# Optimization experiments

Hardware: AMD Instinct MI355X
Metric: run time of the kernel (lower is better)

## Reference

```python
import jax, jax.numpy as jnp
import numpy as np

N = 50000
E = 800000
D_IN = 256
D_OUT = 256
ALPHA = 0.5


def setup_inputs() -> dict:
    key = jax.random.key(0)
    k1, k2, k3, k4, k5, k6 = jax.random.split(key, 6)
    stdv = 1.0 / np.sqrt(D_OUT)
    return {
        "input": jax.random.normal(k1, (N, D_IN), dtype=jnp.float32),
        "adj_src": jax.random.randint(k2, (E,), 0, N, dtype=jnp.int64),
        "adj_dst": jax.random.randint(k3, (E,), 0, N, dtype=jnp.int64),
        "adj_w": jax.random.uniform(k4, (E,), dtype=jnp.float32),
        "init_input": jax.random.normal(k5, (N, D_OUT), dtype=jnp.float32),
        "weight": jax.random.uniform(k6, (D_IN, D_OUT), dtype=jnp.float32,
                                     minval=-stdv, maxval=stdv),
    }


def reference(input, adj_src, adj_dst, adj_w, init_input, weight):
    # support = input @ W          [N, D_OUT] (dense GEMM)
    support = jnp.matmul(input, weight)
    # spmm: out[dst] += w * support[src]   (COO aggregate)
    msgs = support[adj_src] * adj_w[:, None]          # [E, D_OUT]
    agg = jax.ops.segment_sum(msgs, adj_dst, num_segments=N)  # [N, D_OUT]
    # alpha-blended residual + ReLU (bias=False, act=ReLU)
    out = agg * ALPHA + init_input * (1.0 - ALPHA)
    return jax.nn.relu(out)
```

## Files before the change

### kernel.cpp

```cpp
#include <hip/hip_runtime.h>
#include <hip/hip_fp16.h>

#define ALPHA 0.5f

typedef short short8v __attribute__((ext_vector_type(8)));
typedef float f32x4 __attribute__((ext_vector_type(4)));

__device__ __forceinline__ unsigned short f2bf(float f) {
  union { float f; unsigned u; } v; v.f = f;
  unsigned r = v.u + 0x7FFFu + ((v.u >> 16) & 1u);
  return (unsigned short)(r >> 16);
}
__device__ __forceinline__ float bf2f(unsigned short u) {
  union { unsigned u; float f; } v; v.u = ((unsigned)u) << 16;
  return v.f;
}
__device__ __forceinline__ float unpack_w(unsigned p) {
  return __half2float(__ushort_as_half((unsigned short)((p & 0x7FFFu) << 1)));
}

__global__ __launch_bounds__(256) void prep_small(
    const float* __restrict__ W, unsigned short* __restrict__ Wt,
    int* __restrict__ deg, int* __restrict__ scanmeta, int N) {
  const int tid = threadIdx.x;
  const int bid = blockIdx.x;
  if (bid < 256) {
    __shared__ float tile[16][17];
    const int kb = (bid & 15) * 16, nb = (bid >> 4) * 16;
    const int tx = tid & 15, ty = tid >> 4;
    tile[ty][tx] = W[(kb + ty) * 256 + nb + tx];
    __syncthreads();
    Wt[(nb + ty) * 256 + kb + tx] = f2bf(tile[tx][ty]);
  } else {
    if (bid == 256 && tid < 128) scanmeta[tid] = 0;
    const int base = ((bid - 256) * 256 + tid) * 4;
    if (base + 3 < N) *reinterpret_cast<int4*>(&deg[base]) = make_int4(0, 0, 0, 0);
    else for (int j = 0; j < 4; ++j) if (base + j < N) deg[base + j] = 0;
  }
}

__global__ __launch_bounds__(256) void gemm_hist(
    const float* __restrict__ A, const unsigned short* __restrict__ Wt,
    unsigned short* __restrict__ C, int M,
    const int* __restrict__ dst, int* __restrict__ deg, int E,
    const float* __restrict__ init, unsigned short* __restrict__ init_bf, int n8i,
    int GB, int HB, int CB) {
  __shared__ char smem[2][24576];
  const int tid = threadIdx.x;
  const int bid = blockIdx.x;

  if (bid >= GB + HB) {
    const int cgid = (bid - GB - HB) * 256 + tid;
    const int cstride = CB * 256;
    for (int i = cgid; i < n8i; i += cstride) {
      float4 a = *reinterpret_cast<const float4*>(&init[i * 8]);
      float4 b = *reinterpret_cast<const float4*>(&init[i * 8 + 4]);
      unsigned short o[8] = {
        f2bf(a.x * (1.f - ALPHA)), f2bf(a.y * (1.f - ALPHA)),
        f2bf(a.z * (1.f - ALPHA)), f2bf(a.w * (1.f - ALPHA)),
        f2bf(b.x * (1.f - ALPHA)), f2bf(b.y * (1.f - ALPHA)),
        f2bf(b.z * (1.f - ALPHA)), f2bf(b.w * (1.f - ALPHA))};
      *reinterpret_cast<short8v*>(&init_bf[i * 8]) = *reinterpret_cast<short8v*>(o);
    }
    return;
  }
  if (bid >= GB) {
    const int hgid = (bid - GB) * 256 + tid;
    const int hstride = HB * 256;
    const int E4 = E & ~3;
    for (int i = hgid * 4; i < E4; i += hstride * 4) {
      int4 d = *reinterpret_cast<const int4*>(&dst[i]);
      atomicAdd(&deg[d.x], 1); atomicAdd(&deg[d.y], 1);
      atomicAdd(&deg[d.z], 1); atomicAdd(&deg[d.w], 1);
    }
    if (hgid < (E - E4)) atomicAdd(&deg[dst[E4 + hgid]], 1);
    return;
  }

  const int lane = tid & 63;
  const int w = tid >> 6;
  const int wm = w >> 1, wn = w & 1;
  const int row0 = bid * 128;

  f32x4 acc[4][8];
  #pragma unroll
  for (int m = 0; m < 4; ++m)
    #pragma unroll
    for (int n = 0; n < 8; ++n) acc[m][n] = (f32x4){0.f, 0.f, 0.f, 0.f};

  const int aR = tid >> 1;
  const int aKs = (tid & 1) * 16;
  const int aRow = (row0 + aR < M) ? (row0 + aR) : (M - 1);
  const float* aP = A + (size_t)aRow * 256 + aKs;
  const int aWrOff = (aR >> 4) * 1024 + (aKs >> 3) * 256 + (aR & 15) * 16;

  int cur = 0;
  {
    float4 av[4];
    #pragma unroll
    for (int j = 0; j < 4; ++j) av[j] = *reinterpret_cast<const float4*>(aP + j * 4);
    #pragma unroll
    for (int i = 0; i < 4; ++i) {
      int s = w * 4 + i;
      const unsigned short* g = Wt + (size_t)(s * 16 + (lane & 15)) * 256 + (lane >> 4) * 8;
      __builtin_amdgcn_global_load_lds(
          (const __attribute__((address_space(1))) void*)g,
          (__attribute__((address_space(3))) void*)(&smem[0][8192 + s * 1024]),
          16, 0, 0);
    }
    unsigned short ab[16];
    #pragma unroll
    for (int j = 0; j < 4; ++j) {
      ab[j * 4 + 0] = f2bf(av[j].x); ab[j * 4 + 1] = f2bf(av[j].y);
      ab[j * 4 + 2] = f2bf(av[j].z); ab[j * 4 + 3] = f2bf(av[j].w);
    }
    *reinterpret_cast<short8v*>(&smem[0][aWrOff])       = *reinterpret_cast<short8v*>(&ab[0]);
    *reinterpret_cast<short8v*>(&smem[0][aWrOff + 256]) = *reinterpret_cast<short8v*>(&ab[8]);
    __syncthreads();
  }

  #pragma unroll
  for (int t = 0; t < 8; ++t) {
    float4 av[4];
    const bool pf = (t < 7);
    if (pf) {
      const int k0 = (t + 1) * 32;
      #pragma unroll
      for (int j = 0; j < 4; ++j) av[j] = *reinterpret_cast<const float4*>(aP + k0 + j * 4);
      #pragma unroll
      for (int i = 0; i < 4; ++i) {
        int s = w * 4 + i;
        const unsigned short* g = Wt + (size_t)(s * 16 + (lane & 15)) * 256 + k0 + (lane >> 4) * 8;
        __builtin_amdgcn_global_load_lds(
            (const __attribute__((address_space(1))) void*)g,
            (__attribute__((address_space(3))) void*)(&smem[cur ^ 1][8192 + s * 1024]),
            16, 0, 0);
      }
    }
    short8v af[4], bfv[8];
    #pragma unroll
    for (int m = 0; m < 4; ++m)
      af[m] = *reinterpret_cast<const short8v*>(&smem[cur][(wm * 4 + m) * 1024 + lane * 16]);
    #pragma unroll
    for (int n = 0; n < 8; ++n)
      bfv[n] = *reinterpret_cast<const short8v*>(&smem[cur][8192 + (wn * 8 + n) * 1024 + lane * 16]);
    #pragma unroll
    for (int m = 0; m < 4; ++m)
      #pragma unroll
      for (int n = 0; n < 8; ++n)
        acc[m][n] = __builtin_amdgcn_mfma_f32_16x16x32_bf16(af[m], bfv[n], acc[m][n], 0, 0, 0);
    if (pf) {
      unsigned short ab[16];
      #pragma unroll
      for (int j = 0; j < 4; ++j) {
        ab[j * 4 + 0] = f2bf(av[j].x); ab[j * 4 + 1] = f2bf(av[j].y);
        ab[j * 4 + 2] = f2bf(av[j].z); ab[j * 4 + 3] = f2bf(av[j].w);
      }
      *reinterpret_cast<short8v*>(&smem[cur ^ 1][aWrOff])       = *reinterpret_cast<short8v*>(&ab[0]);
      *reinterpret_cast<short8v*>(&smem[cur ^ 1][aWrOff + 256]) = *reinterpret_cast<short8v*>(&ab[8]);
    }
    __syncthreads();
    cur ^= 1;
  }

  #pragma unroll
  for (int m = 0; m < 4; ++m) {
    #pragma unroll
    for (int n = 0; n < 8; ++n) {
      const int col = wn * 128 + n * 16 + (lane & 15);
      #pragma unroll
      for (int r = 0; r < 4; ++r) {
        const int row = row0 + wm * 64 + m * 16 + (lane >> 4) * 4 + r;
        if (row < M) C[(size_t)row * 256 + col] = f2bf(acc[m][n][r]);
      }
    }
  }
}

__global__ __launch_bounds__(256) void scan_lookback(
    const int* __restrict__ deg, int* __restrict__ row_ptr, int* __restrict__ cursor,
    int* __restrict__ scanmeta ,
    int N, int E, int NB) {
  int* flags = scanmeta;
  int* aggv  = scanmeta + 64;
  const int tid = threadIdx.x;
  const int bid = blockIdx.x;
  const int base = bid * 1024 + tid * 4;

  int4 v = make_int4(0, 0, 0, 0);
  if (base + 3 < N) v = *reinterpret_cast<const int4*>(&deg[base]);
  else {
    if (base + 0 < N) v.x = deg[base + 0];
    if (base + 1 < N) v.y = deg[base + 1];
    if (base + 2 < N) v.z = deg[base + 2];
  }
  const int s = v.x + v.y + v.z + v.w;
  const int lane = tid & 63, wid = tid >> 6;
  int ps = s;
  #pragma unroll
  for (int off = 1; off < 64; off <<= 1) {
    int t = __shfl_up(ps, off, 64);
    if (lane >= off) ps += t;
  }
  __shared__ int wsum[4];
  __shared__ int s_off;
  if (lane == 63) wsum[wid] = ps;
  __syncthreads();
  int woff = 0;
  #pragma unroll
  for (int w2 = 0; w2 < 4; ++w2) woff += (w2 < wid) ? wsum[w2] : 0;
  const int texcl = woff + ps - s;

  if (tid == 0) {
    int total = wsum[0] + wsum[1] + wsum[2] + wsum[3];
    atomicExch(&aggv[bid], total);
    __threadfence();
    atomicExch(&flags[bid], 1);
  }
  if (bid == 0 && tid == 0) row_ptr[N] = E;

  if (tid < 64) {
    int a = 0;
    if (tid < bid) {
      while (atomicAdd(&flags[tid], 0) == 0) { }
      a = atomicAdd(&aggv[tid], 0);
    }
    #pragma unroll
    for (int m = 1; m < 64; m <<= 1) a += __shfl_xor(a, m, 64);
    if (tid == 0) s_off = a;
  }
  __syncthreads();
  const int off = s_off;

  int4 e = make_int4(texcl + off, texcl + off + v.x,
                     texcl + off + v.x + v.y, texcl + off + v.x + v.y + v.z);
  if (base + 3 < N) {
    *reinterpret_cast<int4*>(&row_ptr[base]) = e;
    *reinterpret_cast<int4*>(&cursor[base]) = e;
  } else {
    int ev[4] = {e.x, e.y, e.z, e.w};
    for (int j = 0; j < 4; ++j)
      if (base + j < N) { row_ptr[base + j] = ev[j]; cursor[base + j] = ev[j]; }
  }
}

__global__ __launch_bounds__(256) void reindex_edges(
    const int* __restrict__ src, const int* __restrict__ dst,
    const float* __restrict__ w, int* __restrict__ cursor,
    unsigned* __restrict__ edges, int E) {
  int i = (blockIdx.x * blockDim.x + threadIdx.x) * 4;
  if (i + 3 < E) {
    int4 sv = *reinterpret_cast<const int4*>(&src[i]);
    int4 dv = *reinterpret_cast<const int4*>(&dst[i]);
    float4 wv = *reinterpret_cast<const float4*>(&w[i]);
    int s_[4] = {sv.x, sv.y, sv.z, sv.w};
    int d_[4] = {dv.x, dv.y, dv.z, dv.w};
    float w_[4] = {wv.x, wv.y, wv.z, wv.w};
    #pragma unroll
    for (int j = 0; j < 4; ++j) {
      int slot = atomicAdd(&cursor[d_[j]], 1);
      unsigned hb = __half_as_ushort(__float2half(w_[j] * ALPHA));
      edges[slot] = ((unsigned)s_[j] << 15) | (hb >> 1);
    }
  } else {
    for (; i < E; ++i) {
      int slot = atomicAdd(&cursor[dst[i]], 1);
      unsigned hb = __half_as_ushort(__float2half(w[i] * ALPHA));
      edges[slot] = ((unsigned)src[i] << 15) | (hb >> 1);
    }
  }
}

__global__ __launch_bounds__(256) void aggregate(
    const unsigned short* __restrict__ support,
    const int* __restrict__ row_ptr,
    const unsigned* __restrict__ edges,
    const unsigned short* __restrict__ init_bf, float* __restrict__ out, int N) {
  int node = blockIdx.x * 4 + (threadIdx.x >> 6);
  if (node >= N) return;
  int lane = threadIdx.x & 63;
  int start = row_ptr[node];
  int cnt = row_ptr[node + 1] - start;

  ushort4 ib = *reinterpret_cast<const ushort4*>(&init_bf[(size_t)node * 256 + lane * 4]);

  float4 acc = make_float4(0.f, 0.f, 0.f, 0.f);
  int e = 0;
  for (; e + 7 < cnt; e += 8) {
    unsigned p[8];
    #pragma unroll
    for (int j = 0; j < 8; ++j) p[j] = edges[start + e + j];
    ushort4 v[8];
    #pragma unroll
    for (int j = 0; j < 8; ++j)
      v[j] = *reinterpret_cast<const ushort4*>(&support[(size_t)(p[j] >> 15) * 256 + lane * 4]);
    #pragma unroll
    for (int j = 0; j < 8; ++j) {
      float wj = unpack_w(p[j]);
      acc.x += wj * bf2f(v[j].x);
      acc.y += wj * bf2f(v[j].y);
      acc.z += wj * bf2f(v[j].z);
      acc.w += wj * bf2f(v[j].w);
    }
  }
  for (; e < cnt; ++e) {
    unsigned p = edges[start + e];
    ushort4 v = *reinterpret_cast<const ushort4*>(&support[(size_t)(p >> 15) * 256 + lane * 4]);
    float wj = unpack_w(p);
    acc.x += wj * bf2f(v.x); acc.y += wj * bf2f(v.y);
    acc.z += wj * bf2f(v.z); acc.w += wj * bf2f(v.w);
  }
  float4 o;
  o.x = fmaxf(acc.x + bf2f(ib.x), 0.f);
  o.y = fmaxf(acc.y + bf2f(ib.y), 0.f);
  o.z = fmaxf(acc.z + bf2f(ib.z), 0.f);
  o.w = fmaxf(acc.w + bf2f(ib.w), 0.f);
  *reinterpret_cast<float4*>(&out[(size_t)node * 256 + lane * 4]) = o;
}

extern "C" void kernel_launch(void* const* d_in, const int* in_sizes, int n_in,
                              void* d_out, int out_size, void* d_ws, size_t ws_size,
                              hipStream_t stream) {
  const float* input   = (const float*)d_in[0];
  const int*   adj_src = (const int*)d_in[1];
  const int*   adj_dst = (const int*)d_in[2];
  const float* adj_w   = (const float*)d_in[3];
  const float* init_in = (const float*)d_in[4];
  const float* weight  = (const float*)d_in[5];
  float* out = (float*)d_out;

  const int N = in_sizes[0] / 256;
  const int E = in_sizes[1];

  char* ws = (char*)d_ws;
  unsigned short* support = (unsigned short*)ws; ws += (size_t)N * 256 * 2;
  unsigned short* init_bf = (unsigned short*)ws; ws += (size_t)N * 256 * 2;
  unsigned short* Wt      = (unsigned short*)ws; ws += 256 * 256 * 2;
  int* deg      = (int*)ws; ws += (size_t)N * 4;
  int* row_ptr  = (int*)ws; ws += (size_t)(N + 1) * 4;
  int* cursor   = (int*)ws; ws += (size_t)N * 4;
  int* scanmeta = (int*)ws; ws += 128 * 4;
  unsigned* edges = (unsigned*)ws; ws += (size_t)E * 4;

  const int NB = (N + 1023) / 1024;
  const int GB = (N + 127) / 128;
  const int HB = 640;
  const int CB = 320;
  const int n8i = N * 256 / 8;

  prep_small<<<256 + (N / 4 + 255) / 256, 256, 0, stream>>>(weight, Wt, deg, scanmeta, N);

  gemm_hist<<<GB + HB + CB, 256, 0, stream>>>(input, Wt, support, N,
                                              adj_dst, deg, E,
                                              init_in, init_bf, n8i, GB, HB, CB);

  scan_lookback<<<NB, 256, 0, stream>>>(deg, row_ptr, cursor, scanmeta, N, E, NB);

  reindex_edges<<<(E / 4 + 255) / 256, 256, 0, stream>>>(adj_src, adj_dst, adj_w, cursor, edges, E);

  aggregate<<<(N + 3) / 4, 256, 0, stream>>>(support, row_ptr, edges, init_bf, out, N);
}
```

Before: 193.7 us.

## Move GEMM from histogram kernel to co-run with edge reindexing

Result: faster. 189.1 us (-2.4%).

```diff
diff --git a/kernel.cpp b/kernel.cpp
--- a/kernel.cpp
+++ b/kernel.cpp
@@ -39,33 +39,15 @@
   }
 }
 
-__global__ __launch_bounds__(256) void gemm_hist(
-    const float* __restrict__ A, const unsigned short* __restrict__ Wt,
-    unsigned short* __restrict__ C, int M,
+__global__ __launch_bounds__(256) void hist_cvt(
     const int* __restrict__ dst, int* __restrict__ deg, int E,
     const float* __restrict__ init, unsigned short* __restrict__ init_bf, int n8i,
-    int GB, int HB, int CB) {
-  __shared__ char smem[2][24576];
+    int HB, int CB) {
   const int tid = threadIdx.x;
   const int bid = blockIdx.x;
 
-  if (bid >= GB + HB) {
-    const int cgid = (bid - GB - HB) * 256 + tid;
-    const int cstride = CB * 256;
-    for (int i = cgid; i < n8i; i += cstride) {
-      float4 a = *reinterpret_cast<const float4*>(&init[i * 8]);
-      float4 b = *reinterpret_cast<const float4*>(&init[i * 8 + 4]);
-      unsigned short o[8] = {
-        f2bf(a.x * (1.f - ALPHA)), f2bf(a.y * (1.f - ALPHA)),
-        f2bf(a.z * (1.f - ALPHA)), f2bf(a.w * (1.f - ALPHA)),
-        f2bf(b.x * (1.f - ALPHA)), f2bf(b.y * (1.f - ALPHA)),
-        f2bf(b.z * (1.f - ALPHA)), f2bf(b.w * (1.f - ALPHA))};
-      *reinterpret_cast<short8v*>(&init_bf[i * 8]) = *reinterpret_cast<short8v*>(o);
-    }
-    return;
-  }
-  if (bid >= GB) {
-    const int hgid = (bid - GB) * 256 + tid;
+  if (bid < HB) {
+    const int hgid = bid * 256 + tid;
     const int hstride = HB * 256;
     const int E4 = E & ~3;
     for (int i = hgid * 4; i < E4; i += hstride * 4) {
@@ -76,104 +58,17 @@
     if (hgid < (E - E4)) atomicAdd(&deg[dst[E4 + hgid]], 1);
     return;
   }
-
-  const int lane = tid & 63;
-  const int w = tid >> 6;
-  const int wm = w >> 1, wn = w & 1;
-  const int row0 = bid * 128;
-
-  f32x4 acc[4][8];
-  #pragma unroll
-  for (int m = 0; m < 4; ++m)
-    #pragma unroll
-    for (int n = 0; n < 8; ++n) acc[m][n] = (f32x4){0.f, 0.f, 0.f, 0.f};
-
-  const int aR = tid >> 1;
-  const int aKs = (tid & 1) * 16;
-  const int aRow = (row0 + aR < M) ? (row0 + aR) : (M - 1);
-  const float* aP = A + (size_t)aRow * 256 + aKs;
-  const int aWrOff = (aR >> 4) * 1024 + (aKs >> 3) * 256 + (aR & 15) * 16;
-
-  int cur = 0;
-  {
-    float4 av[4];
-    #pragma unroll
-    for (int j = 0; j < 4; ++j) av[j] = *reinterpret_cast<const float4*>(aP + j * 4);
-    #pragma unroll
-    for (int i = 0; i < 4; ++i) {
-      int s = w * 4 + i;
-      const unsigned short* g = Wt + (size_t)(s * 16 + (lane & 15)) * 256 + (lane >> 4) * 8;
-      __builtin_amdgcn_global_load_lds(
-          (const __attribute__((address_space(1))) void*)g,
-          (__attribute__((address_space(3))) void*)(&smem[0][8192 + s * 1024]),
-          16, 0, 0);
-    }
-    unsigned short ab[16];
-    #pragma unroll
-    for (int j = 0; j < 4; ++j) {
-      ab[j * 4 + 0] = f2bf(av[j].x); ab[j * 4 + 1] = f2bf(av[j].y);
-      ab[j * 4 + 2] = f2bf(av[j].z); ab[j * 4 + 3] = f2bf(av[j].w);
-    }
-    *reinterpret_cast<short8v*>(&smem[0][aWrOff])       = *reinterpret_cast<short8v*>(&ab[0]);
-    *reinterpret_cast<short8v*>(&smem[0][aWrOff + 256]) = *reinterpret_cast<short8v*>(&ab[8]);
-    __syncthreads();
-  }
-
-  #pragma unroll
-  for (int t = 0; t < 8; ++t) {
-    float4 av[4];
-    const bool pf = (t < 7);
-    if (pf) {
-      const int k0 = (t + 1) * 32;
-      #pragma unroll
-      for (int j = 0; j < 4; ++j) av[j] = *reinterpret_cast<const float4*>(aP + k0 + j * 4);
-      #pragma unroll
-      for (int i = 0; i < 4; ++i) {
-        int s = w * 4 + i;
-        const unsigned short* g = Wt + (size_t)(s * 16 + (lane & 15)) * 256 + k0 + (lane >> 4) * 8;
-        __builtin_amdgcn_global_load_lds(
-            (const __attribute__((address_space(1))) void*)g,
-            (__attribute__((address_space(3))) void*)(&smem[cur ^ 1][8192 + s * 1024]),
-            16, 0, 0);
-      }
-    }
-    short8v af[4], bfv[8];
-    #pragma unroll
-    for (int m = 0; m < 4; ++m)
-      af[m] = *reinterpret_cast<const short8v*>(&smem[cur][(wm * 4 + m) * 1024 + lane * 16]);
-    #pragma unroll
-    for (int n = 0; n < 8; ++n)
-      bfv[n] = *reinterpret_cast<const short8v*>(&smem[cur][8192 + (wn * 8 + n) * 1024 + lane * 16]);
-    #pragma unroll
-    for (int m = 0; m < 4; ++m)
-      #pragma unroll
-      for (int n = 0; n < 8; ++n)
-        acc[m][n] = __builtin_amdgcn_mfma_f32_16x16x32_bf16(af[m], bfv[n], acc[m][n], 0, 0, 0);
-    if (pf) {
-      unsigned short ab[16];
-      #pragma unroll
-      for (int j = 0; j < 4; ++j) {
-        ab[j * 4 + 0] = f2bf(av[j].x); ab[j * 4 + 1] = f2bf(av[j].y);
-        ab[j * 4 + 2] = f2bf(av[j].z); ab[j * 4 + 3] = f2bf(av[j].w);
-      }
-      *reinterpret_cast<short8v*>(&smem[cur ^ 1][aWrOff])       = *reinterpret_cast<short8v*>(&ab[0]);
-      *reinterpret_cast<short8v*>(&smem[cur ^ 1][aWrOff + 256]) = *reinterpret_cast<short8v*>(&ab[8]);
-    }
-    __syncthreads();
-    cur ^= 1;
-  }
-
-  #pragma unroll
-  for (int m = 0; m < 4; ++m) {
-    #pragma unroll
-    for (int n = 0; n < 8; ++n) {
-      const int col = wn * 128 + n * 16 + (lane & 15);
-      #pragma unroll
-      for (int r = 0; r < 4; ++r) {
-        const int row = row0 + wm * 64 + m * 16 + (lane >> 4) * 4 + r;
-        if (row < M) C[(size_t)row * 256 + col] = f2bf(acc[m][n][r]);
-      }
-    }
+  const int cgid = (bid - HB) * 256 + tid;
+  const int cstride = CB * 256;
+  for (int i = cgid; i < n8i; i += cstride) {
+    float4 a = *reinterpret_cast<const float4*>(&init[i * 8]);
+    float4 b = *reinterpret_cast<const float4*>(&init[i * 8 + 4]);
+    unsigned short o[8] = {
+      f2bf(a.x * (1.f - ALPHA)), f2bf(a.y * (1.f - ALPHA)),
+      f2bf(a.z * (1.f - ALPHA)), f2bf(a.w * (1.f - ALPHA)),
+      f2bf(b.x * (1.f - ALPHA)), f2bf(b.y * (1.f - ALPHA)),
+      f2bf(b.z * (1.f - ALPHA)), f2bf(b.w * (1.f - ALPHA))};
+    *reinterpret_cast<short8v*>(&init_bf[i * 8]) = *reinterpret_cast<short8v*>(o);
   }
 }
 
@@ -244,29 +139,138 @@
   }
 }
 
-__global__ __launch_bounds__(256) void reindex_edges(
+__global__ __launch_bounds__(256) void gemm_reindex(
+    const float* __restrict__ A, const unsigned short* __restrict__ Wt,
+    unsigned short* __restrict__ C, int M,
     const int* __restrict__ src, const int* __restrict__ dst,
-    const float* __restrict__ w, int* __restrict__ cursor,
-    unsigned* __restrict__ edges, int E) {
-  int i = (blockIdx.x * blockDim.x + threadIdx.x) * 4;
-  if (i + 3 < E) {
-    int4 sv = *reinterpret_cast<const int4*>(&src[i]);
-    int4 dv = *reinterpret_cast<const int4*>(&dst[i]);
-    float4 wv = *reinterpret_cast<const float4*>(&w[i]);
-    int s_[4] = {sv.x, sv.y, sv.z, sv.w};
-    int d_[4] = {dv.x, dv.y, dv.z, dv.w};
-    float w_[4] = {wv.x, wv.y, wv.z, wv.w};
+    const float* __restrict__ wgt, int* __restrict__ cursor,
+    unsigned* __restrict__ edges, int E, int GB, int RB) {
+  __shared__ char smem[2][24576];
+  const int tid = threadIdx.x;
+  const int bid = blockIdx.x;
+
+  if (bid >= GB) {
+    const int rbid = bid - GB;
+    int i = (rbid * 256 + tid) * 4;
+    if (i + 3 < E) {
+      int4 sv = *reinterpret_cast<const int4*>(&src[i]);
+      int4 dv = *reinterpret_cast<const int4*>(&dst[i]);
+      float4 wv = *reinterpret_cast<const float4*>(&wgt[i]);
+      int s_[4] = {sv.x, sv.y, sv.z, sv.w};
+      int d_[4] = {dv.x, dv.y, dv.z, dv.w};
+      float w_[4] = {wv.x, wv.y, wv.z, wv.w};
+      #pragma unroll
+      for (int j = 0; j < 4; ++j) {
+        int slot = atomicAdd(&cursor[d_[j]], 1);
+        unsigned hb = __half_as_ushort(__float2half(w_[j] * ALPHA));
+        edges[slot] = ((unsigned)s_[j] << 15) | (hb >> 1);
+      }
+    } else {
+      for (; i < E; ++i) {
+        int slot = atomicAdd(&cursor[dst[i]], 1);
+        unsigned hb = __half_as_ushort(__float2half(wgt[i] * ALPHA));
+        edges[slot] = ((unsigned)src[i] << 15) | (hb >> 1);
+      }
+    }
+    return;
+  }
+
+  const int lane = tid & 63;
+  const int w = tid >> 6;
+  const int wm = w >> 1, wn = w & 1;
+  const int row0 = bid * 128;
+
+  f32x4 acc[4][8];
+  #pragma unroll
+  for (int m = 0; m < 4; ++m)
+    #pragma unroll
+    for (int n = 0; n < 8; ++n) acc[m][n] = (f32x4){0.f, 0.f, 0.f, 0.f};
+
+  const int aR = tid >> 1;
+  const int aKs = (tid & 1) * 16;
+  const int aRow = (row0 + aR < M) ? (row0 + aR) : (M - 1);
+  const float* aP = A + (size_t)aRow * 256 + aKs;
+  const int aWrOff = (aR >> 4) * 1024 + (aKs >> 3) * 256 + (aR & 15) * 16;
+
+  int cur = 0;
+  {
+    float4 av[4];
+    #pragma unroll
+    for (int j = 0; j < 4; ++j) av[j] = *reinterpret_cast<const float4*>(aP + j * 4);
+    #pragma unroll
+    for (int i = 0; i < 4; ++i) {
+      int s = w * 4 + i;
+      const unsigned short* g = Wt + (size_t)(s * 16 + (lane & 15)) * 256 + (lane >> 4) * 8;
+      __builtin_amdgcn_global_load_lds(
+          (const __attribute__((address_space(1))) void*)g,
+          (__attribute__((address_space(3))) void*)(&smem[0][8192 + s * 1024]),
+          16, 0, 0);
+    }
+    unsigned short ab[16];
     #pragma unroll
     for (int j = 0; j < 4; ++j) {
-      int slot = atomicAdd(&cursor[d_[j]], 1);
-      unsigned hb = __half_as_ushort(__float2half(w_[j] * ALPHA));
-      edges[slot] = ((unsigned)s_[j] << 15) | (hb >> 1);
-    }
-  } else {
-    for (; i < E; ++i) {
-      int slot = atomicAdd(&cursor[dst[i]], 1);
-      unsigned hb = __half_as_ushort(__float2half(w[i] * ALPHA));
-      edges[slot] = ((unsigned)src[i] << 15) | (hb >> 1);
+      ab[j * 4 + 0] = f2bf(av[j].x); ab[j * 4 + 1] = f2bf(av[j].y);
+      ab[j * 4 + 2] = f2bf(av[j].z); ab[j * 4 + 3] = f2bf(av[j].w);
+    }
+    *reinterpret_cast<short8v*>(&smem[0][aWrOff])       = *reinterpret_cast<short8v*>(&ab[0]);
+    *reinterpret_cast<short8v*>(&smem[0][aWrOff + 256]) = *reinterpret_cast<short8v*>(&ab[8]);
+    __syncthreads();
+  }
+
+  #pragma unroll
+  for (int t = 0; t < 8; ++t) {
+    float4 av[4];
+    const bool pf = (t < 7);
+    if (pf) {
+      const int k0 = (t + 1) * 32;
+      #pragma unroll
+      for (int j = 0; j < 4; ++j) av[j] = *reinterpret_cast<const float4*>(aP + k0 + j * 4);
+      #pragma unroll
+      for (int i = 0; i < 4; ++i) {
+        int s = w * 4 + i;
+        const unsigned short* g = Wt + (size_t)(s * 16 + (lane & 15)) * 256 + k0 + (lane >> 4) * 8;
+        __builtin_amdgcn_global_load_lds(
+            (const __attribute__((address_space(1))) void*)g,
+            (__attribute__((address_space(3))) void*)(&smem[cur ^ 1][8192 + s * 1024]),
+            16, 0, 0);
+      }
+    }
+    short8v af[4], bfv[8];
+    #pragma unroll
+    for (int m = 0; m < 4; ++m)
+      af[m] = *reinterpret_cast<const short8v*>(&smem[cur][(wm * 4 + m) * 1024 + lane * 16]);
+    #pragma unroll
+    for (int n = 0; n < 8; ++n)
+      bfv[n] = *reinterpret_cast<const short8v*>(&smem[cur][8192 + (wn * 8 + n) * 1024 + lane * 16]);
+    #pragma unroll
+    for (int m = 0; m < 4; ++m)
+      #pragma unroll
+      for (int n = 0; n < 8; ++n)
+        acc[m][n] = __builtin_amdgcn_mfma_f32_16x16x32_bf16(af[m], bfv[n], acc[m][n], 0, 0, 0);
+    if (pf) {
+      unsigned short ab[16];
+      #pragma unroll
+      for (int j = 0; j < 4; ++j) {
+        ab[j * 4 + 0] = f2bf(av[j].x); ab[j * 4 + 1] = f2bf(av[j].y);
+        ab[j * 4 + 2] = f2bf(av[j].z); ab[j * 4 + 3] = f2bf(av[j].w);
+      }
+      *reinterpret_cast<short8v*>(&smem[cur ^ 1][aWrOff])       = *reinterpret_cast<short8v*>(&ab[0]);
+      *reinterpret_cast<short8v*>(&smem[cur ^ 1][aWrOff + 256]) = *reinterpret_cast<short8v*>(&ab[8]);
+    }
+    __syncthreads();
+    cur ^= 1;
+  }
+
+  #pragma unroll
+  for (int m = 0; m < 4; ++m) {
+    #pragma unroll
+    for (int n = 0; n < 8; ++n) {
+      const int col = wn * 128 + n * 16 + (lane & 15);
+      #pragma unroll
+      for (int r = 0; r < 4; ++r) {
+        const int row = row0 + wm * 64 + m * 16 + (lane >> 4) * 4 + r;
+        if (row < M) C[(size_t)row * 256 + col] = f2bf(acc[m][n][r]);
+      }
     }
   }
 }
@@ -343,20 +347,21 @@
   unsigned* edges = (unsigned*)ws; ws += (size_t)E * 4;
 
   const int NB = (N + 1023) / 1024;
+  const int HB = 800;
+  const int CB = 512;
   const int GB = (N + 127) / 128;
-  const int HB = 640;
-  const int CB = 320;
+  const int RB = (E / 4 + 255) / 256;
   const int n8i = N * 256 / 8;
 
   prep_small<<<256 + (N / 4 + 255) / 256, 256, 0, stream>>>(weight, Wt, deg, scanmeta, N);
 
-  gemm_hist<<<GB + HB + CB, 256, 0, stream>>>(input, Wt, support, N,
-                                              adj_dst, deg, E,
-                                              init_in, init_bf, n8i, GB, HB, CB);
+  hist_cvt<<<HB + CB, 256, 0, stream>>>(adj_dst, deg, E, init_in, init_bf, n8i, HB, CB);
 
   scan_lookback<<<NB, 256, 0, stream>>>(deg, row_ptr, cursor, scanmeta, N, E, NB);
 
-  reindex_edges<<<(E / 4 + 255) / 256, 256, 0, stream>>>(adj_src, adj_dst, adj_w, cursor, edges, E);
+  gemm_reindex<<<GB + RB, 256, 0, stream>>>(input, Wt, support, N,
+                                            adj_src, adj_dst, adj_w, cursor,
+                                            edges, E, GB, RB);
 
   aggregate<<<(N + 3) / 4, 256, 0, stream>>>(support, row_ptr, edges, init_bf, out, N);
 }
```
